# Performance work log

Hardware: AMD Instinct MI355X
Metric: run time of the kernel (lower is better)

The kernel has to match this reference:

```python
import jax, jax.numpy as jnp
import numpy as np

B, T, C = 4, 1024, 768
NH = 12
HD = C // NH  # 64


def setup_inputs() -> dict:
    key = jax.random.key(0)
    k1, k2, k3, k4, k5 = jax.random.split(key, 5)
    s = 0.02
    return {
        "x": jax.random.normal(k1, (B, T, C), dtype=jnp.float32),
        "Wqkv": jax.random.normal(k2, (C, 3 * C), dtype=jnp.float32) * s,
        "bqkv": jax.random.normal(k3, (3 * C,), dtype=jnp.float32) * s,
        "Wproj": jax.random.normal(k4, (C, C), dtype=jnp.float32) * s,
        "bproj": jax.random.normal(k5, (C,), dtype=jnp.float32) * s,
        "start_pos": 0,
    }


def reference(x, Wqkv, bqkv, Wproj, bproj, start_pos):
    # Manual QKV projection (nn.Linear with weight stored as [in, out])
    Bq, Tq, Cq = x.shape
    qkv = x @ Wqkv + bqkv                       # [B, T, 3C]
    q, k, v = jnp.split(qkv, 3, axis=-1)
    q = q.reshape(Bq, Tq, NH, HD)
    k = k.reshape(Bq, Tq, NH, HD)
    v = v.reshape(Bq, Tq, NH, HD)
    # With start_pos=0 the KV-cache write+slice is an identity on k, v.
    att = jnp.einsum("bqhd,bkhd->bhqk", q, k) / jnp.sqrt(jnp.float32(HD))
    causal = jnp.tril(jnp.ones((Tq, Tq), dtype=bool))  # [T, T]
    att = jnp.where(causal[None, None], att, jnp.float32(-jnp.inf))
    att = jax.nn.softmax(att, axis=-1)
    out = jnp.einsum("bhqk,bkhd->bqhd", att, v).reshape(Bq, Tq, Cq)
    return out @ Wproj + bproj
```

## Files before the change

kernel.cpp:

```cpp
#include <hip/hip_runtime.h>


#define BB 4
#define TT 1024
#define CC 768
#define NHH 12
#define HDD 64
#define BHH (BB*NHH)

typedef unsigned short u16;
typedef __attribute__((ext_vector_type(8))) short bf16x8;
typedef __attribute__((ext_vector_type(4))) float f32x4;
typedef __attribute__((ext_vector_type(4))) int i32x4;

__device__ __forceinline__ u16 f2b(float f) {
  unsigned u = __float_as_uint(f);
  u += 0x7fffu + ((u >> 16) & 1u);
  return (u16)(u >> 16);
}
__device__ __forceinline__ unsigned packbf(float lo, float hi) {
  return (__float_as_uint(hi) & 0xffff0000u) | (__float_as_uint(lo) >> 16);
}

__device__ __forceinline__ void gload_lds16(const u16* g, u16* l) {
  __builtin_amdgcn_global_load_lds(
      (const __attribute__((address_space(1))) unsigned int*)g,
      (__attribute__((address_space(3))) unsigned int*)l, 16, 0, 0);
}

__device__ __forceinline__ void tr_body(const float* __restrict__ in, u16* __restrict__ out,
                                        int R, int Cc, int bx, int by, float (*tile)[33]) {
  int c0 = bx * 32, r0 = by * 32;
  int tx = threadIdx.x & 31, ty = threadIdx.x >> 5;
#pragma unroll
  for (int i = 0; i < 32; i += 8)
    tile[ty + i][tx] = in[(r0 + ty + i) * Cc + c0 + tx];
  __syncthreads();
#pragma unroll
  for (int i = 0; i < 32; i += 8)
    out[(c0 + ty + i) * R + r0 + tx] = f2b(tile[tx][ty + i]);
}

__global__ __launch_bounds__(256) void k_prep(const float* __restrict__ x, u16* __restrict__ xb,
                                              const float* __restrict__ Wqkv, u16* __restrict__ Wqkv_t,
                                              const float* __restrict__ Wproj, u16* __restrict__ Wproj_t) {
  __shared__ float tile[32][33];
  int bid = blockIdx.x;
  if (bid < 3072) {
    int i = bid * 256 + threadIdx.x;
    float4 v = ((const float4*)x)[i];
    ushort4 o;
    o.x = f2b(v.x); o.y = f2b(v.y); o.z = f2b(v.z); o.w = f2b(v.w);
    ((ushort4*)xb)[i] = o;
  } else if (bid < 3072 + 1728) {
    int tb = bid - 3072;
    tr_body(Wqkv, Wqkv_t, CC, 3 * CC, tb % 72, tb / 72, tile);
  } else {
    int tb = bid - 4800;
    tr_body(Wproj, Wproj_t, CC, CC, tb % 24, tb / 24, tile);
  }
}


#define STAGE7(k0_, Ad_, Bd_)                                                     \
  _Pragma("unroll") for (int i_ = 0; i_ < 4; i_++)                                \
    gload_lds16(ga + i_ * 32 * CC + (k0_), (Ad_) + i_ * 2048 + tid * 8);          \
  _Pragma("unroll") for (int i_ = 0; i_ < 3; i_++)                                \
    gload_lds16(gb + i_ * 32 * CC + (k0_), (Bd_) + i_ * 2048 + tid * 8);

#define COMPUTE96(As_, Bs_)                                                       \
  { bf16x8 af[4][2], bfr[3][2];                                                   \
    _Pragma("unroll") for (int i = 0; i < 4; i++) {                               \
      const u16* ar = (As_) + (wm + i * 16 + id16) * 64;                          \
      af[i][0] = *(const bf16x8*)(ar + off0);                                     \
      af[i][1] = *(const bf16x8*)(ar + off1);                                     \
    }                                                                             \
    _Pragma("unroll") for (int j = 0; j < 3; j++) {                               \
      const u16* br = (Bs_) + (wn48 + j * 16 + id16) * 64;                        \
      bfr[j][0] = *(const bf16x8*)(br + off0);                                    \
      bfr[j][1] = *(const bf16x8*)(br + off1);                                    \
    }                                                                             \
    _Pragma("unroll") for (int i = 0; i < 4; i++)                                 \
      _Pragma("unroll") for (int j = 0; j < 3; j++) {                             \
        acc[i][j] = __builtin_amdgcn_mfma_f32_16x16x32_bf16(af[i][0], bfr[j][0],  \
                                                            acc[i][j], 0, 0, 0);  \
        acc[i][j] = __builtin_amdgcn_mfma_f32_16x16x32_bf16(af[i][1], bfr[j][1],  \
                                                            acc[i][j], 0, 0, 0);  \
      } }

#define GEMM_CORE96_DB(A_, Bt_, m0_, n0_, SMEM)                                   \
  u16* As0 = (SMEM);          u16* Bs0 = (SMEM) + 8192;                           \
  u16* As1 = (SMEM) + 14336;  u16* Bs1 = (SMEM) + 22528;                          \
  int tid = threadIdx.x;                                                          \
  int wave = tid >> 6, lane = tid & 63, quad = lane >> 4, id16 = lane & 15;       \
  int wm = (wave & 1) * 64, wn48 = (wave >> 1) * 48;                              \
  int srow = tid >> 3;                                                            \
  int schunk = (tid & 7) ^ (srow & 7);                                            \
  const u16* ga = A_ + (m0_ + srow) * CC + schunk * 8;                            \
  const u16* gb = Bt_ + (n0_ + srow) * CC + schunk * 8;                           \
  int xk = id16 & 7;                                                              \
  int off0 = (quad ^ xk) * 8, off1 = ((4 + quad) ^ xk) * 8;                       \
  f32x4 acc[4][3];                                                                \
  _Pragma("unroll") for (int i = 0; i < 4; i++)                                   \
      _Pragma("unroll") for (int j = 0; j < 3; j++) acc[i][j] = (f32x4){0,0,0,0}; \
  STAGE7(0, As0, Bs0)                                                             \
  for (int kk = 0; kk < 6; kk++) {                                                \
    int kA = kk * 128;                                                            \
                               \
    STAGE7(kA + 64, As1, Bs1)                                                     \
    asm volatile("s_waitcnt vmcnt(7)" ::: "memory");                              \
    __builtin_amdgcn_s_barrier();                                                 \
    asm volatile("" ::: "memory");                                                \
    COMPUTE96(As0, Bs0)                                                           \
    __builtin_amdgcn_s_barrier();                                                 \
    asm volatile("" ::: "memory");                                                \
             \
    if (kk < 5) {                                                                 \
      STAGE7(kA + 128, As0, Bs0)                                                  \
      asm volatile("s_waitcnt vmcnt(7)" ::: "memory");                            \
    } else {                                                                      \
      asm volatile("s_waitcnt vmcnt(0)" ::: "memory");                            \
    }                                                                             \
    __builtin_amdgcn_s_barrier();                                                 \
    asm volatile("" ::: "memory");                                                \
    COMPUTE96(As1, Bs1)                                                           \
    __builtin_amdgcn_s_barrier();                                                 \
    asm volatile("" ::: "memory");                                                \
  }

__global__ __launch_bounds__(256) void k_qkv(const u16* __restrict__ A, const u16* __restrict__ Bt,
                                             const float* __restrict__ bias,
                                             u16* __restrict__ Qb, u16* __restrict__ Kb,
                                             u16* __restrict__ Vt) {
  __shared__ u16 smem[28672];
  int xcd = blockIdx.x & 7, g = blockIdx.x >> 3;
  int m0 = (xcd + 8 * (g / 24)) * 128, n0 = (g % 24) * 96;
  GEMM_CORE96_DB(A, Bt, m0, n0, smem)
  float bv[3];
#pragma unroll
  for (int j = 0; j < 3; j++) bv[j] = bias[n0 + wn48 + j * 16 + id16];
  int bi = m0 >> 10, t0 = m0 & 1023;

  if (n0 < 2 * CC) {
    u16* dstb = (n0 < CC) ? Qb : Kb;
    int nrel0 = (n0 < CC) ? n0 : n0 - CC;
#pragma unroll
    for (int i = 0; i < 4; i++)
#pragma unroll
      for (int j = 0; j < 3; j++)
#pragma unroll
        for (int r = 0; r < 4; r++)
          smem[(wm + i * 16 + quad * 4 + r) * 104 + wn48 + j * 16 + id16] =
              f2b(acc[i][j][r] + bv[j]);
    __syncthreads();
#pragma unroll
    for (int u = tid; u < 384; u += 256) {
      int row = u / 3, seg = u % 3;
      int ng = nrel0 + seg * 32;
      int h = ng >> 6, d0 = ng & 63;
      const u16* src = smem + row * 104 + seg * 32;
      u16* dst = dstb + ((bi * NHH + h) * TT + t0 + row) * HDD + d0;
#pragma unroll
      for (int w2 = 0; w2 < 4; w2++)
        ((bf16x8*)dst)[w2] = ((const bf16x8*)src)[w2];
    }
  } else {
#pragma unroll
    for (int i = 0; i < 4; i++)
#pragma unroll
      for (int j = 0; j < 3; j++)
#pragma unroll
        for (int r = 0; r < 4; r++)
          smem[(wn48 + j * 16 + id16) * 136 + wm + i * 16 + quad * 4 + r] =
              f2b(acc[i][j][r] + bv[j]);
    __syncthreads();
    if (tid < 192) {
      int row = tid >> 1, mseg = tid & 1;
      int dd = n0 - 2 * CC + row;
      int h = dd >> 6, d = dd & 63;
      const u16* src = smem + row * 136 + mseg * 64;
      u16* dst = Vt + ((bi * NHH + h) * HDD + d) * TT + t0 + mseg * 64;
#pragma unroll
      for (int w2 = 0; w2 < 8; w2++)
        ((bf16x8*)dst)[w2] = ((const bf16x8*)src)[w2];
    }
  }
}

__global__ __launch_bounds__(256) void k_proj(const u16* __restrict__ A, const u16* __restrict__ Bt,
                                              const float* __restrict__ bias, float* __restrict__ out) {
  __shared__ u16 smem[28672];
  int xcd = blockIdx.x & 7, g = blockIdx.x >> 3;
  int m0 = (xcd + 8 * (g / 8)) * 128, n0 = (g % 8) * 96;
  GEMM_CORE96_DB(A, Bt, m0, n0, smem)
  float bv[3];
#pragma unroll
  for (int j = 0; j < 3; j++) bv[j] = bias[n0 + wn48 + j * 16 + id16];
#pragma unroll
  for (int i = 0; i < 4; i++) {
#pragma unroll
    for (int j = 0; j < 3; j++) {
#pragma unroll
      for (int r = 0; r < 4; r++) {
        int m = m0 + wm + i * 16 + quad * 4 + r;
        int n = n0 + wn48 + j * 16 + id16;
        out[m * CC + n] = acc[i][j][r] + bv[j];
      }
    }
  }
}

__global__ __launch_bounds__(128) void k_attn(const u16* __restrict__ Qb, const u16* __restrict__ Kb,
                                              const u16* __restrict__ Vt, u16* __restrict__ Ob) {
  __shared__ __align__(16) u16 Ks[2][64 * 64];
  __shared__ __align__(16) u16 Vs[2][64 * 64];
  int tid = threadIdx.x;
  int wave = tid >> 6, lane = tid & 63, quad = lane >> 4, id16 = lane & 15;
  int bh = blockIdx.x % BHH, t = 15 - (blockIdx.x / BHH);
  int b = bh / NHH, h = bh % NHH;
  int qw = t * 64 + wave * 32;
  int nch = t + 1;
  const float cexp = 0.125f * 1.44269504088896f;
  bf16x8 bones;
#pragma unroll
  for (int e = 0; e < 8; e++) bones[e] = (short)0x3F80;

  const u16* Kg = Kb + (bh * TT) * HDD;
  const u16* Vg = Vt + (bh * HDD) * TT;
  int srow = tid >> 3;
  int schunk = (tid & 7) ^ (srow & 7);

  int xk = id16 & 7;
  int koff0 = (quad ^ xk) * 8;
  int koff1 = ((quad + 4) ^ xk) * 8;
  int half = (quad & 1) * 4;
  int voff0 = (((quad >> 1)) ^ xk) * 8 + half;
  int voff1 = (((quad >> 1) + 2) ^ xk) * 8 + half;
  int voff2 = (((quad >> 1) + 4) ^ xk) * 8 + half;
  int voff3 = (((quad >> 1) + 6) ^ xk) * 8 + half;

  bf16x8 aq[2][2];
#pragma unroll
  for (int rh = 0; rh < 2; rh++) {
    const u16* Qrow = Qb + (bh * TT + qw + 16 * rh + id16) * HDD;
    aq[rh][0] = *(const bf16x8*)(Qrow + quad * 8);
    aq[rh][1] = *(const bf16x8*)(Qrow + 32 + quad * 8);
  }
  f32x4 o[2][4], ol[2];
#pragma unroll
  for (int rh = 0; rh < 2; rh++) {
    ol[rh] = (f32x4){0,0,0,0};
#pragma unroll
    for (int dt = 0; dt < 4; dt++) o[rh][dt] = (f32x4){0,0,0,0};
  }

#pragma unroll
  for (int i = 0; i < 4; i++) {
    gload_lds16(Kg + (16 * i + srow) * HDD + schunk * 8, Ks[0] + i * 1024 + tid * 8);
    gload_lds16(Vg + (16 * i + srow) * TT + schunk * 8, Vs[0] + i * 1024 + tid * 8);
  }

  for (int c = 0; c < nch; c++) {
    __syncthreads();
    if (c + 1 < nch) {
      int kb = (c + 1) * 64;
      u16* kd = Ks[(c + 1) & 1];
      u16* vd = Vs[(c + 1) & 1];
#pragma unroll
      for (int i = 0; i < 4; i++) {
        gload_lds16(Kg + (kb + 16 * i + srow) * HDD + schunk * 8, kd + i * 1024 + tid * 8);
        gload_lds16(Vg + (16 * i + srow) * TT + kb + schunk * 8, vd + i * 1024 + tid * 8);
      }
    }
    const u16* kbuf = Ks[c & 1];
    const u16* vbuf = Vs[c & 1];
    bool diag = (c == nch - 1);
    int kb = c * 64;

    bf16x8 kf0[4], kf1[4];
#pragma unroll
    for (int kt = 0; kt < 4; kt++) {
      const u16* kr = kbuf + (kt * 16 + id16) * 64;
      kf0[kt] = *(const bf16x8*)(kr + koff0);
      kf1[kt] = *(const bf16x8*)(kr + koff1);
    }
    bf16x8 vf0[4], vf1[4];
#pragma unroll
    for (int dt = 0; dt < 4; dt++) {
      const u16* vr = vbuf + (dt * 16 + id16) * 64;
      uint2 a0 = *(const uint2*)(vr + voff0);
      uint2 a1 = *(const uint2*)(vr + voff1);
      uint2 a2 = *(const uint2*)(vr + voff2);
      uint2 a3 = *(const uint2*)(vr + voff3);
      i32x4 w0, w1;
      w0.x = a0.x; w0.y = a0.y; w0.z = a1.x; w0.w = a1.y;
      w1.x = a2.x; w1.y = a2.y; w1.z = a3.x; w1.w = a3.y;
      vf0[dt] = __builtin_bit_cast(bf16x8, w0);
      vf1[dt] = __builtin_bit_cast(bf16x8, w1);
    }

#pragma unroll
    for (int rh = 0; rh < 2; rh++) {
      f32x4 st[4];
#pragma unroll
      for (int kt = 0; kt < 4; kt++) {
        f32x4 z = {0,0,0,0};
        z = __builtin_amdgcn_mfma_f32_16x16x32_bf16(kf0[kt], aq[rh][0], z, 0, 0, 0);
        st[kt] = __builtin_amdgcn_mfma_f32_16x16x32_bf16(kf1[kt], aq[rh][1], z, 0, 0, 0);
      }
      unsigned pk[4][2];
      if (!diag) {
#pragma unroll
        for (int kt = 0; kt < 4; kt++) {
          pk[kt][0] = packbf(__builtin_amdgcn_exp2f(st[kt][0] * cexp),
                             __builtin_amdgcn_exp2f(st[kt][1] * cexp));
          pk[kt][1] = packbf(__builtin_amdgcn_exp2f(st[kt][2] * cexp),
                             __builtin_amdgcn_exp2f(st[kt][3] * cexp));
        }
      } else {
        int qrow = qw + 16 * rh + id16;
#pragma unroll
        for (int kt = 0; kt < 4; kt++) {
          float pv[4];
#pragma unroll
          for (int r = 0; r < 4; r++) {
            int key = kb + kt * 16 + quad * 4 + r;
            float p = __builtin_amdgcn_exp2f(st[kt][r] * cexp);
            pv[r] = (key <= qrow) ? p : 0.f;
          }
          pk[kt][0] = packbf(pv[0], pv[1]);
          pk[kt][1] = packbf(pv[2], pv[3]);
        }
      }
      i32x4 b0v, b1v;
      b0v.x = (int)pk[0][0]; b0v.y = (int)pk[0][1];
      b0v.z = (int)pk[1][0]; b0v.w = (int)pk[1][1];
      b1v.x = (int)pk[2][0]; b1v.y = (int)pk[2][1];
      b1v.z = (int)pk[3][0]; b1v.w = (int)pk[3][1];
      bf16x8 pf0 = __builtin_bit_cast(bf16x8, b0v);
      bf16x8 pf1 = __builtin_bit_cast(bf16x8, b1v);

#pragma unroll
      for (int dt = 0; dt < 4; dt++) {
        o[rh][dt] = __builtin_amdgcn_mfma_f32_16x16x32_bf16(vf0[dt], pf0, o[rh][dt], 0, 0, 0);
        o[rh][dt] = __builtin_amdgcn_mfma_f32_16x16x32_bf16(vf1[dt], pf1, o[rh][dt], 0, 0, 0);
      }
      ol[rh] = __builtin_amdgcn_mfma_f32_16x16x32_bf16(bones, pf0, ol[rh], 0, 0, 0);
      ol[rh] = __builtin_amdgcn_mfma_f32_16x16x32_bf16(bones, pf1, ol[rh], 0, 0, 0);
    }
  }

#pragma unroll
  for (int rh = 0; rh < 2; rh++) {
    float inv = 1.0f / ol[rh][0];
    int qg = qw + 16 * rh + id16;
    u16* dst = Ob + (b * TT + qg) * CC + h * HDD + quad * 4;
#pragma unroll
    for (int dt = 0; dt < 4; dt++) {
      unsigned lo = ((unsigned)f2b(o[rh][dt][1] * inv) << 16) | f2b(o[rh][dt][0] * inv);
      unsigned hi = ((unsigned)f2b(o[rh][dt][3] * inv) << 16) | f2b(o[rh][dt][2] * inv);
      uint2 pairv; pairv.x = lo; pairv.y = hi;
      *(uint2*)(dst + dt * 16) = pairv;
    }
  }
}

extern "C" void kernel_launch(void* const* d_in, const int* in_sizes, int n_in,
                              void* d_out, int out_size, void* d_ws, size_t ws_size,
                              hipStream_t stream) {
  const float* x     = (const float*)d_in[0];
  const float* Wqkv  = (const float*)d_in[1];
  const float* bqkv  = (const float*)d_in[2];
  const float* Wproj = (const float*)d_in[3];
  const float* bproj = (const float*)d_in[4];
  float* out = (float*)d_out;

  u16* ws = (u16*)d_ws;
  u16* xb      = ws;
  u16* Wqkv_t  = xb + BB * TT * CC;
  u16* Wproj_t = Wqkv_t + 3 * CC * CC;
  u16* Qb      = Wproj_t + CC * CC;
  u16* Kb      = Qb + BHH * TT * HDD;
  u16* Vt      = Kb + BHH * TT * HDD;
  u16* Ob      = Vt + BHH * TT * HDD;

  k_prep<<<3072 + 1728 + 576, 256, 0, stream>>>(x, xb, Wqkv, Wqkv_t, Wproj, Wproj_t);
  k_qkv<<<32 * 24, 256, 0, stream>>>(xb, Wqkv_t, bqkv, Qb, Kb, Vt);
  k_attn<<<16 * BHH, 128, 0, stream>>>(Qb, Kb, Vt, Ob);
  k_proj<<<32 * 8, 256, 0, stream>>>(Ob, Wproj_t, bproj, out);
}
```

Baseline: 132.5 us.

## Load K/V MFMA fragments directly from global memory instead of LDS staging

```diff
diff --git a/kernel.cpp b/kernel.cpp
--- a/kernel.cpp
+++ b/kernel.cpp
@@ -212,8 +212,6 @@
 
 __global__ __launch_bounds__(128) void k_attn(const u16* __restrict__ Qb, const u16* __restrict__ Kb,
                                               const u16* __restrict__ Vt, u16* __restrict__ Ob) {
-  __shared__ __align__(16) u16 Ks[2][64 * 64];
-  __shared__ __align__(16) u16 Vs[2][64 * 64];
   int tid = threadIdx.x;
   int wave = tid >> 6, lane = tid & 63, quad = lane >> 4, id16 = lane & 15;
   int bh = blockIdx.x % BHH, t = 15 - (blockIdx.x / BHH);
@@ -227,17 +225,6 @@
 
   const u16* Kg = Kb + (bh * TT) * HDD;
   const u16* Vg = Vt + (bh * HDD) * TT;
-  int srow = tid >> 3;
-  int schunk = (tid & 7) ^ (srow & 7);
-
-  int xk = id16 & 7;
-  int koff0 = (quad ^ xk) * 8;
-  int koff1 = ((quad + 4) ^ xk) * 8;
-  int half = (quad & 1) * 4;
-  int voff0 = (((quad >> 1)) ^ xk) * 8 + half;
-  int voff1 = (((quad >> 1) + 2) ^ xk) * 8 + half;
-  int voff2 = (((quad >> 1) + 4) ^ xk) * 8 + half;
-  int voff3 = (((quad >> 1) + 6) ^ xk) * 8 + half;
 
   bf16x8 aq[2][2];
 #pragma unroll
@@ -254,44 +241,25 @@
     for (int dt = 0; dt < 4; dt++) o[rh][dt] = (f32x4){0,0,0,0};
   }
 
-#pragma unroll
-  for (int i = 0; i < 4; i++) {
-    gload_lds16(Kg + (16 * i + srow) * HDD + schunk * 8, Ks[0] + i * 1024 + tid * 8);
-    gload_lds16(Vg + (16 * i + srow) * TT + schunk * 8, Vs[0] + i * 1024 + tid * 8);
-  }
-
   for (int c = 0; c < nch; c++) {
-    __syncthreads();
-    if (c + 1 < nch) {
-      int kb = (c + 1) * 64;
-      u16* kd = Ks[(c + 1) & 1];
-      u16* vd = Vs[(c + 1) & 1];
-#pragma unroll
-      for (int i = 0; i < 4; i++) {
-        gload_lds16(Kg + (kb + 16 * i + srow) * HDD + schunk * 8, kd + i * 1024 + tid * 8);
-        gload_lds16(Vg + (16 * i + srow) * TT + kb + schunk * 8, vd + i * 1024 + tid * 8);
-      }
-    }
-    const u16* kbuf = Ks[c & 1];
-    const u16* vbuf = Vs[c & 1];
     bool diag = (c == nch - 1);
     int kb = c * 64;
 
     bf16x8 kf0[4], kf1[4];
 #pragma unroll
     for (int kt = 0; kt < 4; kt++) {
-      const u16* kr = kbuf + (kt * 16 + id16) * 64;
-      kf0[kt] = *(const bf16x8*)(kr + koff0);
-      kf1[kt] = *(const bf16x8*)(kr + koff1);
+      const u16* kr = Kg + (kb + kt * 16 + id16) * HDD + quad * 8;
+      kf0[kt] = *(const bf16x8*)(kr);
+      kf1[kt] = *(const bf16x8*)(kr + 32);
     }
     bf16x8 vf0[4], vf1[4];
 #pragma unroll
     for (int dt = 0; dt < 4; dt++) {
-      const u16* vr = vbuf + (dt * 16 + id16) * 64;
-      uint2 a0 = *(const uint2*)(vr + voff0);
-      uint2 a1 = *(const uint2*)(vr + voff1);
-      uint2 a2 = *(const uint2*)(vr + voff2);
-      uint2 a3 = *(const uint2*)(vr + voff3);
+      const u16* vb = Vg + (dt * 16 + id16) * TT + kb + (quad >> 1) * 8 + (quad & 1) * 4;
+      uint2 a0 = *(const uint2*)(vb);
+      uint2 a1 = *(const uint2*)(vb + 16);
+      uint2 a2 = *(const uint2*)(vb + 32);
+      uint2 a3 = *(const uint2*)(vb + 48);
       i32x4 w0, w1;
       w0.x = a0.x; w0.y = a0.y; w0.z = a1.x; w0.w = a1.y;
       w1.x = a2.x; w1.y = a2.y; w1.z = a3.x; w1.w = a3.y;
```

After: 159.2 us. 1.2x slower.
